# Kernel tuning notes

Measured on AMD Instinct MI355X. Metric: run time of the kernel, lower is better.

The kernel has to match this reference:

```python
import jax, jax.numpy as jnp
import numpy as np

H = 8        # num attention heads
DH = 160     # head dim (hidden_size // H)
HS = 1280    # hidden_size
CAD = 768    # cross_attention_dim
R = 4        # LoRA rank
LORA_SCALE = 1.0  # `scale` forward arg (default 1.0)


def setup_inputs() -> dict:
    key = jax.random.key(0)
    ks = jax.random.split(key, 16)
    rn = lambda k, s, std=0.02: (jax.random.normal(k, s) * std).astype(jnp.float32)
    return {
        "hidden_states": jax.random.normal(ks[0], (8, 4096, HS), jnp.float32),
        "encoder_hidden_states": jax.random.normal(ks[1], (8, 77, CAD), jnp.float32),
        # base attention projections (nn.Linear weight layout: [out, in])
        "Wq": rn(ks[2], (HS, HS)),
        "Wk": rn(ks[3], (HS, CAD)),
        "Wv": rn(ks[4], (HS, CAD)),
        "Wo": rn(ks[5], (HS, HS)),
        "bo": jnp.zeros((HS,), jnp.float32),
        # LoRA down/up pairs (down std ~ 1/rank; up nonzero so grads flow)
        "q_down": rn(ks[6], (R, HS), 0.25), "q_up": rn(ks[7], (HS, R)),
        "k_down": rn(ks[8], (R, CAD), 0.25), "k_up": rn(ks[9], (HS, R)),
        "v_down": rn(ks[10], (R, CAD), 0.25), "v_up": rn(ks[11], (HS, R)),
        "o_down": rn(ks[12], (R, HS), 0.25), "o_up": rn(ks[13], (HS, R)),
    }


def reference(hidden_states, encoder_hidden_states, Wq, Wk, Wv, Wo, bo,
              q_down, q_up, k_down, k_up, v_down, v_up, o_down, o_up):
    B, S, _ = hidden_states.shape
    T = encoder_hidden_states.shape[1]
    lora = lambda x, d, u: (x @ d.T) @ u.T  # LoRALinearLayer: up(down(x))

    q = hidden_states @ Wq.T + LORA_SCALE * lora(hidden_states, q_down, q_up)
    k = encoder_hidden_states @ Wk.T + LORA_SCALE * lora(encoder_hidden_states, k_down, k_up)
    v = encoder_hidden_states @ Wv.T + LORA_SCALE * lora(encoder_hidden_states, v_down, v_up)

    q = q.reshape(B, S, H, DH)
    k = k.reshape(B, T, H, DH)
    v = v.reshape(B, T, H, DH)

    # attn.get_attention_scores: scaled QK^T, softmax (no mask)
    inv_sqrt_d = jnp.asarray(1.0 / np.sqrt(DH), q.dtype)
    scores = jnp.einsum('bshd,bthd->bhst', q, k) * inv_sqrt_d
    probs = jax.nn.softmax(scores, axis=-1)
    o = jnp.einsum('bhst,bthd->bshd', probs, v).reshape(B, S, H * DH)

    # to_out[0] (Linear with bias) + LoRA on the same input; to_out[1] dropout = identity (eval)
    return o @ Wo.T + bo + LORA_SCALE * lora(o, o_down, o_up)
```

## Files before the change

### kernel.cpp

```cpp
#include <hip/hip_runtime.h>
#include <hip/hip_bf16.h>
#include <stdint.h>

typedef short bf16x8 __attribute__((ext_vector_type(8)));
typedef float f32x4 __attribute__((ext_vector_type(4)));

#define DEVI static __device__ __forceinline__

DEVI ushort f2bf(float f) {
  union { float f; uint32_t u; } v; v.f = f;
  uint32_t u = v.u;
  return (ushort)((u + 0x7fffu + ((u >> 16) & 1u)) >> 16);
}

DEVI void gload16(const void* g, void* l) {
  __builtin_amdgcn_global_load_lds((const __attribute__((address_space(1))) void*)g,
                                   (__attribute__((address_space(3))) void*)l,
                                   16, 0, 0);
}

#define SB() __builtin_amdgcn_sched_barrier(0)
#define BAR() __builtin_amdgcn_s_barrier()
#define MFMA(a, b, c) __builtin_amdgcn_mfma_f32_16x16x32_bf16((a), (b), (c), 0, 0, 0)


__global__ void fold_kernel(const float* __restrict__ W, const float* __restrict__ up,
                            const float* __restrict__ down, ushort* __restrict__ out,
                            int OUT, int IN, int transpose, float scale) {
  int idx = blockIdx.x * 256 + threadIdx.x;
  if (idx >= OUT * IN) return;
  int o = idx / IN, i = idx % IN;
  float v = W[idx];
#pragma unroll
  for (int r = 0; r < 4; ++r) v += up[o * 4 + r] * down[r * IN + i];
  v *= scale;
  out[transpose ? ((long)i * OUT + o) : idx] = f2bf(v);
}

__global__ void cvt_kernel(const float* __restrict__ in, ushort* __restrict__ out, int n8) {
  int idx = blockIdx.x * 256 + threadIdx.x;
  if (idx >= n8) return;
  const float4* p = (const float4*)(in + (long)idx * 8);
  float4 a = p[0], b = p[1];
  union { ushort us[8]; uint4 v; } r;
  r.us[0] = f2bf(a.x); r.us[1] = f2bf(a.y); r.us[2] = f2bf(a.z); r.us[3] = f2bf(a.w);
  r.us[4] = f2bf(b.x); r.us[5] = f2bf(b.y); r.us[6] = f2bf(b.z); r.us[7] = f2bf(b.w);
  *(uint4*)(out + (long)idx * 8) = r.v;
}


__global__ __launch_bounds__(256) void gemm_bt(
    const ushort* __restrict__ A, long sA0, long sA1, int lda, int validM,
    const ushort* __restrict__ B, long sB0, long sB1, int ldb, int validN,
    float* __restrict__ C32, ushort* __restrict__ C16, long sC0, long sC1, int ldc,
    const float* __restrict__ bias, int K)
{
  __shared__ ushort As[128 * 32];
  __shared__ ushort Bs[128 * 32];

  const int z = blockIdx.z;
  const ushort* Ab = A + (long)(z >> 3) * sA0 + (long)(z & 7) * sA1;
  const ushort* Bb = B + (long)(z >> 3) * sB0 + (long)(z & 7) * sB1;
  const int m0 = blockIdx.x * 128;
  const int n0 = blockIdx.y * 128;
  const int tid = threadIdx.x;
  const int lane = tid & 63;
  const int wid = tid >> 6;

  const int c0 = tid;
  const int arow0 = min(m0 + (c0 >> 2), validM - 1);
  const int arow1 = min(m0 + (c0 >> 2) + 64, validM - 1);
  const int brow0 = min(n0 + (c0 >> 2), validN - 1);
  const int brow1 = min(n0 + (c0 >> 2) + 64, validN - 1);
  const int seg = (c0 & 3) * 8;

  const int wr = (wid >> 1) * 64;
  const int wc = (wid & 1) * 64;
  const int frow = lane & 15;
  const int fk = (lane >> 4) * 8;

  f32x4 acc[4][4] = {};

  for (int kt = 0; kt < K; kt += 32) {
    gload16(Ab + (long)arow0 * lda + kt + seg, As + c0 * 8);
    gload16(Ab + (long)arow1 * lda + kt + seg, As + (c0 + 256) * 8);
    gload16(Bb + (long)brow0 * ldb + kt + seg, Bs + c0 * 8);
    gload16(Bb + (long)brow1 * ldb + kt + seg, Bs + (c0 + 256) * 8);
    __syncthreads();

    bf16x8 af[4], bfr[4];
#pragma unroll
    for (int m = 0; m < 4; ++m)
      af[m] = *(const bf16x8*)(As + (wr + m * 16 + frow) * 32 + fk);
#pragma unroll
    for (int n = 0; n < 4; ++n)
      bfr[n] = *(const bf16x8*)(Bs + (wc + n * 16 + frow) * 32 + fk);
#pragma unroll
    for (int m = 0; m < 4; ++m)
#pragma unroll
      for (int n = 0; n < 4; ++n)
        acc[m][n] = MFMA(af[m], bfr[n], acc[m][n]);
    __syncthreads();
  }

  const long cb = (long)(z >> 3) * sC0 + (long)(z & 7) * sC1;
  const int crow = m0 + wr + (lane >> 4) * 4;
  const int ccol = n0 + wc + (lane & 15);
#pragma unroll
  for (int m = 0; m < 4; ++m)
#pragma unroll
    for (int n = 0; n < 4; ++n)
#pragma unroll
      for (int j = 0; j < 4; ++j) {
        int r = crow + m * 16 + j;
        int c = ccol + n * 16;
        if (r < validM && c < validN) {
          float v = acc[m][n][j];
          if (bias) v += bias[c];
          if (C32) C32[cb + (long)r * ldc + c] = v;
          else     C16[cb + (long)r * ldc + c] = f2bf(v);
        }
      }
}

__global__ __launch_bounds__(256, 2) void score_softmax(
    const ushort* __restrict__ hsb, const ushort* __restrict__ Mt,
    ushort* __restrict__ probs)
{
  __shared__ ushort lds[40960];

  const int z = blockIdx.z;
  const int s0 = blockIdx.x * 128;
  const int h0 = blockIdx.y * 2;
  const int tid = threadIdx.x;
  const int lane = tid & 63;
  const int wid = tid >> 6;
  const int wM = wid >> 1;
  const int wN = wid & 1;
  const int l15 = lane & 15;
  const int l4 = lane >> 4;
  const int sl = tid & 7;

  const ushort* Ag = hsb + ((long)z * 4096 + s0) * 1280;
  long asrc[4]; int adst[4];
#pragma unroll
  for (int j = 0; j < 4; ++j) {
    int r = j * 32 + (tid >> 3);
    asrc[j] = (long)r * 1280 + ((sl ^ (r & 7)) * 8);
    adst[j] = (j * 256 + tid) * 8;
  }
  const ushort* Bg = Mt + (long)z * (640L * 1280);
  long bsrc[6]; int bdst[6];
#pragma unroll
  for (int j = 0; j < 6; ++j) {
    int rb = j * 32 + (tid >> 3);
    int c = h0 * 96 + rb;
    int hh = c / 96, tt = min(c - hh * 96, 76);
    bsrc[j] = (long)(hh * 77 + tt) * 1280 + ((sl ^ (rb & 7)) * 8);
    bdst[j] = 8192 + (j * 256 + tid) * 8;
  }

  int aoff[2][4], boff[2][6];
#pragma unroll
  for (int kk = 0; kk < 2; ++kk) {
#pragma unroll
    for (int m = 0; m < 4; ++m) {
      int r = wM * 64 + m * 16 + l15;
      aoff[kk][m] = r * 64 + (((kk * 4 + l4) ^ (r & 7)) * 8);
    }
#pragma unroll
    for (int n = 0; n < 6; ++n) {
      int r = wN * 96 + n * 16 + l15;
      boff[kk][n] = 8192 + r * 64 + (((kk * 4 + l4) ^ (r & 7)) * 8);
    }
  }

  f32x4 acc[4][6] = {};

#define SS_STAGE(bb, kt) { \
    _Pragma("unroll") for (int j = 0; j < 4; ++j) gload16(Ag + asrc[j] + (kt), &lds[(bb) + adst[j]]); \
    _Pragma("unroll") for (int j = 0; j < 6; ++j) gload16(Bg + bsrc[j] + (kt), &lds[(bb) + bdst[j]]); }

  SS_STAGE(0, 0)

  for (int t = 0; t < 20; ++t) {
    const int base = (t & 1) * 20480;
    if (t + 1 < 20) {
      SS_STAGE(20480 - base, (t + 1) * 64)
      asm volatile("s_waitcnt vmcnt(10)" ::: "memory");
    } else {
      asm volatile("s_waitcnt vmcnt(0)" ::: "memory");
    }
    SB(); BAR(); SB();
#pragma unroll
    for (int kk = 0; kk < 2; ++kk) {
      bf16x8 av[4], bv[6];
#pragma unroll
      for (int m = 0; m < 4; ++m) av[m] = *(const bf16x8*)(&lds[base + aoff[kk][m]]);
#pragma unroll
      for (int n = 0; n < 6; ++n) bv[n] = *(const bf16x8*)(&lds[base + boff[kk][n]]);
      __builtin_amdgcn_s_setprio(1);
#pragma unroll
      for (int m = 0; m < 4; ++m)
#pragma unroll
        for (int n = 0; n < 6; ++n)
          acc[m][n] = MFMA(av[m], bv[n], acc[m][n]);
      __builtin_amdgcn_s_setprio(0);
    }
    SB(); BAR();
  }
#undef SS_STAGE

#pragma unroll
  for (int m = 0; m < 4; ++m)
#pragma unroll
    for (int j = 0; j < 4; ++j) {
      float mx = -1e30f;
#pragma unroll
      for (int n = 0; n < 6; ++n)
        if (n * 16 + l15 < 77) mx = fmaxf(mx, acc[m][n][j]);
#pragma unroll
      for (int o = 8; o; o >>= 1) mx = fmaxf(mx, __shfl_xor(mx, o));
      float sum = 0.f;
#pragma unroll
      for (int n = 0; n < 6; ++n) {
        float e = (n * 16 + l15 < 77) ? __expf(acc[m][n][j] - mx) : 0.f;
        acc[m][n][j] = e;
        sum += e;
      }
#pragma unroll
      for (int o = 8; o; o >>= 1) sum += __shfl_xor(sum, o);
      float inv = 1.f / sum;
#pragma unroll
      for (int n = 0; n < 6; ++n) acc[m][n][j] *= inv;
    }

  __syncthreads();
  ushort* pw = lds + wid * 5632;
#pragma unroll
  for (int m = 0; m < 4; ++m)
#pragma unroll
    for (int n = 0; n < 5; ++n)
#pragma unroll
      for (int j = 0; j < 4; ++j)
        pw[(m * 16 + l4 * 4 + j) * 88 + n * 16 + l15] = f2bf(acc[m][n][j]);

  const uint* pw32 = (const uint*)pw;
  uint* probs32 = (uint*)probs;
  const int head = h0 + wN;
  const long sbase = (long)z * 4096 + s0 + wM * 64;
#pragma unroll 4
  for (int k = 0; k < 40; ++k) {
    int f2 = k * 64 + lane;
    int r = f2 / 40;
    int tp = f2 - r * 40;
    probs32[(sbase + r) * 320 + head * 40 + tp] = pw32[r * 44 + tp];
  }
}

__global__ __launch_bounds__(256, 2) void gemm_out(
    const ushort* __restrict__ P, const ushort* __restrict__ Nt,
    float* __restrict__ C, const float* __restrict__ bias)
{
  __shared__ ushort lds[32768];

  const int z = blockIdx.z;
  const ushort* Ab = P + (long)z * (4096L * 640) + (long)blockIdx.x * 128 * 640;
  const ushort* Bb = Nt + (long)z * (1280L * 640) + (long)blockIdx.y * 128 * 640;
  const int tid = threadIdx.x;
  const int lane = tid & 63;
  const int wid = tid >> 6;
  const int wM = wid >> 1;
  const int wN = wid & 1;
  const int l15 = lane & 15;
  const int l4 = lane >> 4;
  const int sl = tid & 7;

  long asrc[4]; int adst[4], bdst[4];
#pragma unroll
  for (int j = 0; j < 4; ++j) {
    int r = j * 32 + (tid >> 3);
    asrc[j] = (long)r * 640 + ((sl ^ (r & 7)) * 8);
    adst[j] = (j * 256 + tid) * 8;
    bdst[j] = 8192 + (j * 256 + tid) * 8;
  }

  int aoff[2][4], boff[2][4];
#pragma unroll
  for (int kk = 0; kk < 2; ++kk) {
#pragma unroll
    for (int m = 0; m < 4; ++m) {
      int r = wM * 64 + m * 16 + l15;
      aoff[kk][m] = r * 64 + (((kk * 4 + l4) ^ (r & 7)) * 8);
    }
#pragma unroll
    for (int n = 0; n < 4; ++n) {
      int r = wN * 64 + n * 16 + l15;
      boff[kk][n] = 8192 + r * 64 + (((kk * 4 + l4) ^ (r & 7)) * 8);
    }
  }

  f32x4 acc[4][4] = {};

#define OG_STAGE(bb, kt) { \
    _Pragma("unroll") for (int j = 0; j < 4; ++j) gload16(Ab + asrc[j] + (kt), &lds[(bb) + adst[j]]); \
    _Pragma("unroll") for (int j = 0; j < 4; ++j) gload16(Bb + asrc[j] + (kt), &lds[(bb) + bdst[j]]); }

  OG_STAGE(0, 0)

  for (int t = 0; t < 10; ++t) {
    const int base = (t & 1) * 16384;
    if (t + 1 < 10) {
      OG_STAGE(16384 - base, (t + 1) * 64)
      asm volatile("s_waitcnt vmcnt(8)" ::: "memory");
    } else {
      asm volatile("s_waitcnt vmcnt(0)" ::: "memory");
    }
    SB(); BAR(); SB();
#pragma unroll
    for (int kk = 0; kk < 2; ++kk) {
      bf16x8 av[4], bv[4];
#pragma unroll
      for (int m = 0; m < 4; ++m) av[m] = *(const bf16x8*)(&lds[base + aoff[kk][m]]);
#pragma unroll
      for (int n = 0; n < 4; ++n) bv[n] = *(const bf16x8*)(&lds[base + boff[kk][n]]);
      __builtin_amdgcn_s_setprio(1);
#pragma unroll
      for (int m = 0; m < 4; ++m)
#pragma unroll
        for (int n = 0; n < 4; ++n)
          acc[m][n] = MFMA(av[m], bv[n], acc[m][n]);
      __builtin_amdgcn_s_setprio(0);
    }
    SB(); BAR();
  }
#undef OG_STAGE

  __syncthreads();
  float* pw = (float*)lds + wid * 1088;
  const int ccol = blockIdx.y * 128 + wN * 64;
  const float4 bv4 = *(const float4*)(bias + ccol + l15 * 4);
  const long crow0 = (long)z * 4096 + blockIdx.x * 128 + wM * 64;
#pragma unroll
  for (int m = 0; m < 4; ++m) {
#pragma unroll
    for (int n = 0; n < 4; ++n)
#pragma unroll
      for (int j = 0; j < 4; ++j)
        pw[(l4 * 4 + j) * 68 + n * 16 + l15] = acc[m][n][j];
    asm volatile("s_waitcnt lgkmcnt(0)" ::: "memory"); SB();
#pragma unroll
    for (int pass = 0; pass < 4; ++pass) {
      int r = pass * 4 + l4;
      float4 v = *(const float4*)(pw + r * 68 + l15 * 4);
      v.x += bv4.x; v.y += bv4.y; v.z += bv4.z; v.w += bv4.w;
      *(float4*)(C + (crow0 + m * 16 + r) * 1280 + ccol + l15 * 4) = v;
    }
    asm volatile("s_waitcnt lgkmcnt(0)" ::: "memory"); SB();
  }
}

__global__ void zero_nt_pad(ushort* __restrict__ Nt) {
  int idx = blockIdx.x * 256 + threadIdx.x;
  if (idx >= 8 * 1280 * 24) return;
  int b = idx / (1280 * 24);
  int rem = idx % (1280 * 24);
  int j = rem / 24, q = rem % 24;
  int h = q / 3, t = 77 + q % 3;
  Nt[(long)b * 1280 * 640 + (long)j * 640 + h * 80 + t] = 0;
}

extern "C" void kernel_launch(void* const* d_in, const int* in_sizes, int n_in,
                              void* d_out, int out_size, void* d_ws, size_t ws_size,
                              hipStream_t stream) {
  (void)in_sizes; (void)n_in; (void)out_size; (void)ws_size;
  const float* hs     = (const float*)d_in[0];
  const float* ehs    = (const float*)d_in[1];
  const float* Wq     = (const float*)d_in[2];
  const float* Wk     = (const float*)d_in[3];
  const float* Wv     = (const float*)d_in[4];
  const float* Wo     = (const float*)d_in[5];
  const float* bo     = (const float*)d_in[6];
  const float* q_down = (const float*)d_in[7];
  const float* q_up   = (const float*)d_in[8];
  const float* k_down = (const float*)d_in[9];
  const float* k_up   = (const float*)d_in[10];
  const float* v_down = (const float*)d_in[11];
  const float* v_up   = (const float*)d_in[12];
  const float* o_down = (const float*)d_in[13];
  const float* o_up   = (const float*)d_in[14];

  char* w = (char*)d_ws;
  size_t off = 0;
  auto alloc = [&](size_t b) { char* p = w + off; off = (off + b + 255) & ~(size_t)255; return p; };
  ushort* hs_bf  = (ushort*)alloc(32768L * 1280 * 2);
  ushort* ehs_bf = (ushort*)alloc(616L * 768 * 2);
  ushort* WqT    = (ushort*)alloc(1280L * 1280 * 2);
  ushort* Wkv    = (ushort*)alloc(2560L * 768 * 2);
  ushort* Wo_bf  = (ushort*)alloc(1280L * 1280 * 2);
  ushort* kv_bf  = (ushort*)alloc(616L * 2560 * 2);
  ushort* Mt     = (ushort*)alloc(8L * 640 * 1280 * 2);
  ushort* Nt     = (ushort*)alloc(8L * 1280 * 640 * 2);
  ushort* probs  = (ushort*)alloc(8L * 4096 * 640 * 2);
  float*  outp   = (float*)d_out;
  const float invs = 0.07905694150420949f;

  fold_kernel<<<6400, 256, 0, stream>>>(Wq, q_up, q_down, WqT, 1280, 1280, 1, invs);
  fold_kernel<<<3840, 256, 0, stream>>>(Wk, k_up, k_down, Wkv, 1280, 768, 0, 1.0f);
  fold_kernel<<<3840, 256, 0, stream>>>(Wv, v_up, v_down, Wkv + 1280L * 768, 1280, 768, 0, 1.0f);
  fold_kernel<<<6400, 256, 0, stream>>>(Wo, o_up, o_down, Wo_bf, 1280, 1280, 0, 1.0f);
  cvt_kernel<<<20480, 256, 0, stream>>>(hs, hs_bf, 5242880);
  cvt_kernel<<<231, 256, 0, stream>>>(ehs, ehs_bf, 59136);
  gemm_bt<<<dim3(5, 20, 1), 256, 0, stream>>>(ehs_bf, 0, 0, 768, 616,
      Wkv, 0, 0, 768, 2560, nullptr, kv_bf, 0, 0, 2560, nullptr, 768);
  gemm_bt<<<dim3(1, 10, 64), 256, 0, stream>>>(kv_bf, 77L * 2560, 160, 2560, 77,
      WqT, 0, 160, 1280, 1280, nullptr, Mt, 640L * 1280, 77L * 1280, 1280, nullptr, 160);
  gemm_bt<<<dim3(10, 1, 64), 256, 0, stream>>>(Wo_bf, 0, 160, 1280, 1280,
      kv_bf + 1280, 77L * 2560, 160, 2560, 77, nullptr, Nt, 1280L * 640, 80, 640, nullptr, 160);
  zero_nt_pad<<<960, 256, 0, stream>>>(Nt);
  score_softmax<<<dim3(32, 4, 8), 256, 0, stream>>>(hs_bf, Mt, probs);
  gemm_out<<<dim3(32, 10, 8), 256, 0, stream>>>(probs, Nt, outp, bo);
}
```

Baseline: 286.2 us.

## Fuse prep kernels into one launch and halve K-tile in attention GEMMs

Merges the hidden-state and encoder bf16 conversions, the four LoRA weight folds and the Nt pad zeroing into one block-indexed prep kernel. This removes several small kernel launches and their tail gaps. Separately, score_softmax and gemm_out now stage 32-wide K tiles with a 4-way XOR swizzle instead of 64-wide tiles with 8-way, halving LDS use per block. That may allow more resident blocks, but it doubles the number of barrier-synchronized iterations and shrinks the prefetch depth per stage.

Result: faster. 280.6 us (-2.0%).

```diff
diff --git a/kernel.cpp b/kernel.cpp
--- a/kernel.cpp
+++ b/kernel.cpp
@@ -22,30 +22,62 @@
 #define SB() __builtin_amdgcn_sched_barrier(0)
 #define BAR() __builtin_amdgcn_s_barrier()
 #define MFMA(a, b, c) __builtin_amdgcn_mfma_f32_16x16x32_bf16((a), (b), (c), 0, 0, 0)
-
-
-__global__ void fold_kernel(const float* __restrict__ W, const float* __restrict__ up,
-                            const float* __restrict__ down, ushort* __restrict__ out,
-                            int OUT, int IN, int transpose, float scale) {
-  int idx = blockIdx.x * 256 + threadIdx.x;
-  if (idx >= OUT * IN) return;
-  int o = idx / IN, i = idx % IN;
-  float v = W[idx];
-#pragma unroll
-  for (int r = 0; r < 4; ++r) v += up[o * 4 + r] * down[r * IN + i];
-  v *= scale;
-  out[transpose ? ((long)i * OUT + o) : idx] = f2bf(v);
-}
-
-__global__ void cvt_kernel(const float* __restrict__ in, ushort* __restrict__ out, int n8) {
-  int idx = blockIdx.x * 256 + threadIdx.x;
-  if (idx >= n8) return;
-  const float4* p = (const float4*)(in + (long)idx * 8);
-  float4 a = p[0], b = p[1];
-  union { ushort us[8]; uint4 v; } r;
-  r.us[0] = f2bf(a.x); r.us[1] = f2bf(a.y); r.us[2] = f2bf(a.z); r.us[3] = f2bf(a.w);
-  r.us[4] = f2bf(b.x); r.us[5] = f2bf(b.y); r.us[6] = f2bf(b.z); r.us[7] = f2bf(b.w);
-  *(uint4*)(out + (long)idx * 8) = r.v;
+#define KEY4(r) ((((r) & 3)) ^ (((r) >> 2) & 3))
+
+__global__ __launch_bounds__(256) void prep_fused(
+    const float* __restrict__ hs, ushort* __restrict__ hs_bf,
+    const float* __restrict__ ehs, ushort* __restrict__ ehs_bf,
+    const float* __restrict__ Wq, const float* __restrict__ q_up, const float* __restrict__ q_down,
+    ushort* __restrict__ WqT,
+    const float* __restrict__ Wk, const float* __restrict__ k_up, const float* __restrict__ k_down,
+    const float* __restrict__ Wv, const float* __restrict__ v_up, const float* __restrict__ v_down,
+    ushort* __restrict__ Wkv,
+    const float* __restrict__ Wo, const float* __restrict__ o_up, const float* __restrict__ o_down,
+    ushort* __restrict__ Wo_bf,
+    ushort* __restrict__ Nt, float invs)
+{
+  const int b = blockIdx.x;
+  const int tid = threadIdx.x;
+  if (b < 20480) {
+    long idx = (long)b * 256 + tid;
+    const float4* p = (const float4*)(hs + idx * 8);
+    float4 a = p[0], c = p[1];
+    union { ushort us[8]; uint4 v; } r;
+    r.us[0] = f2bf(a.x); r.us[1] = f2bf(a.y); r.us[2] = f2bf(a.z); r.us[3] = f2bf(a.w);
+    r.us[4] = f2bf(c.x); r.us[5] = f2bf(c.y); r.us[6] = f2bf(c.z); r.us[7] = f2bf(c.w);
+    *(uint4*)(hs_bf + idx * 8) = r.v;
+  } else if (b < 20711) {
+    int idx = (b - 20480) * 256 + tid;
+    if (idx < 59136) {
+      const float4* p = (const float4*)(ehs + (long)idx * 8);
+      float4 a = p[0], c = p[1];
+      union { ushort us[8]; uint4 v; } r;
+      r.us[0] = f2bf(a.x); r.us[1] = f2bf(a.y); r.us[2] = f2bf(a.z); r.us[3] = f2bf(a.w);
+      r.us[4] = f2bf(c.x); r.us[5] = f2bf(c.y); r.us[6] = f2bf(c.z); r.us[7] = f2bf(c.w);
+      *(uint4*)(ehs_bf + (long)idx * 8) = r.v;
+    }
+  } else if (b < 41191) {
+    long f = (long)(b - 20711) * 256 + tid;
+    const float *W, *up, *down; ushort* out;
+    int OUT, IN, transpose; float scale; long base;
+    if (f < 1638400)        { base = f;           W = Wq; up = q_up; down = q_down; out = WqT;   OUT = 1280; IN = 1280; transpose = 1; scale = invs; }
+    else if (f < 2621440)   { base = f - 1638400; W = Wk; up = k_up; down = k_down; out = Wkv;   OUT = 1280; IN = 768;  transpose = 0; scale = 1.f; }
+    else if (f < 3604480)   { base = f - 2621440; W = Wv; up = v_up; down = v_down; out = Wkv + 1280L * 768; OUT = 1280; IN = 768; transpose = 0; scale = 1.f; }
+    else                    { base = f - 3604480; W = Wo; up = o_up; down = o_down; out = Wo_bf; OUT = 1280; IN = 1280; transpose = 0; scale = 1.f; }
+    int o = (int)(base / IN), i = (int)(base % IN);
+    float v = W[base];
+#pragma unroll
+    for (int r = 0; r < 4; ++r) v += up[o * 4 + r] * down[r * IN + i];
+    v *= scale;
+    out[transpose ? ((long)i * OUT + o) : base] = f2bf(v);
+  } else {
+    int idx = (b - 41191) * 256 + tid;
+    int bb = idx / (1280 * 24);
+    int rem = idx % (1280 * 24);
+    int j = rem / 24, q = rem % 24;
+    int h = q / 3, t = 77 + q % 3;
+    Nt[(long)bb * 1280 * 640 + (long)j * 640 + h * 80 + t] = 0;
+  }
 }
 
 
@@ -127,7 +159,7 @@
     const ushort* __restrict__ hsb, const ushort* __restrict__ Mt,
     ushort* __restrict__ probs)
 {
-  __shared__ ushort lds[40960];
+  __shared__ ushort lds[22528];
 
   const int z = blockIdx.z;
   const int s0 = blockIdx.x * 128;
@@ -139,74 +171,68 @@
   const int wN = wid & 1;
   const int l15 = lane & 15;
   const int l4 = lane >> 4;
-  const int sl = tid & 7;
+  const int sl = tid & 3;
 
   const ushort* Ag = hsb + ((long)z * 4096 + s0) * 1280;
-  long asrc[4]; int adst[4];
-#pragma unroll
-  for (int j = 0; j < 4; ++j) {
-    int r = j * 32 + (tid >> 3);
-    asrc[j] = (long)r * 1280 + ((sl ^ (r & 7)) * 8);
+  long asrc[2]; int adst[2];
+#pragma unroll
+  for (int j = 0; j < 2; ++j) {
+    int r = j * 64 + (tid >> 2);
+    asrc[j] = (long)r * 1280 + ((sl ^ KEY4(r)) * 8);
     adst[j] = (j * 256 + tid) * 8;
   }
   const ushort* Bg = Mt + (long)z * (640L * 1280);
-  long bsrc[6]; int bdst[6];
-#pragma unroll
-  for (int j = 0; j < 6; ++j) {
-    int rb = j * 32 + (tid >> 3);
+  long bsrc[3]; int bdst[3];
+#pragma unroll
+  for (int j = 0; j < 3; ++j) {
+    int rb = j * 64 + (tid >> 2);
     int c = h0 * 96 + rb;
     int hh = c / 96, tt = min(c - hh * 96, 76);
-    bsrc[j] = (long)(hh * 77 + tt) * 1280 + ((sl ^ (rb & 7)) * 8);
-    bdst[j] = 8192 + (j * 256 + tid) * 8;
-  }
-
-  int aoff[2][4], boff[2][6];
-#pragma unroll
-  for (int kk = 0; kk < 2; ++kk) {
-#pragma unroll
-    for (int m = 0; m < 4; ++m) {
-      int r = wM * 64 + m * 16 + l15;
-      aoff[kk][m] = r * 64 + (((kk * 4 + l4) ^ (r & 7)) * 8);
-    }
-#pragma unroll
-    for (int n = 0; n < 6; ++n) {
-      int r = wN * 96 + n * 16 + l15;
-      boff[kk][n] = 8192 + r * 64 + (((kk * 4 + l4) ^ (r & 7)) * 8);
-    }
+    bsrc[j] = (long)(hh * 77 + tt) * 1280 + ((sl ^ KEY4(rb)) * 8);
+    bdst[j] = 4096 + (j * 256 + tid) * 8;
+  }
+
+  int aoff[4], boff[6];
+#pragma unroll
+  for (int m = 0; m < 4; ++m) {
+    int r = wM * 64 + m * 16 + l15;
+    aoff[m] = r * 32 + ((l4 ^ KEY4(r)) * 8);
+  }
+#pragma unroll
+  for (int n = 0; n < 6; ++n) {
+    int r = wN * 96 + n * 16 + l15;
+    boff[n] = 4096 + r * 32 + ((l4 ^ KEY4(r)) * 8);
   }
 
   f32x4 acc[4][6] = {};
 
 #define SS_STAGE(bb, kt) { \
-    _Pragma("unroll") for (int j = 0; j < 4; ++j) gload16(Ag + asrc[j] + (kt), &lds[(bb) + adst[j]]); \
-    _Pragma("unroll") for (int j = 0; j < 6; ++j) gload16(Bg + bsrc[j] + (kt), &lds[(bb) + bdst[j]]); }
+    _Pragma("unroll") for (int j = 0; j < 2; ++j) gload16(Ag + asrc[j] + (kt), &lds[(bb) + adst[j]]); \
+    _Pragma("unroll") for (int j = 0; j < 3; ++j) gload16(Bg + bsrc[j] + (kt), &lds[(bb) + bdst[j]]); }
 
   SS_STAGE(0, 0)
 
-  for (int t = 0; t < 20; ++t) {
-    const int base = (t & 1) * 20480;
-    if (t + 1 < 20) {
-      SS_STAGE(20480 - base, (t + 1) * 64)
-      asm volatile("s_waitcnt vmcnt(10)" ::: "memory");
+  for (int t = 0; t < 40; ++t) {
+    const int base = (t & 1) * 10240;
+    if (t + 1 < 40) {
+      SS_STAGE(10240 - base, (t + 1) * 32)
+      asm volatile("s_waitcnt vmcnt(5)" ::: "memory");
     } else {
       asm volatile("s_waitcnt vmcnt(0)" ::: "memory");
     }
     SB(); BAR(); SB();
-#pragma unroll
-    for (int kk = 0; kk < 2; ++kk) {
-      bf16x8 av[4], bv[6];
-#pragma unroll
-      for (int m = 0; m < 4; ++m) av[m] = *(const bf16x8*)(&lds[base + aoff[kk][m]]);
-#pragma unroll
-      for (int n = 0; n < 6; ++n) bv[n] = *(const bf16x8*)(&lds[base + boff[kk][n]]);
-      __builtin_amdgcn_s_setprio(1);
-#pragma unroll
-      for (int m = 0; m < 4; ++m)
-#pragma unroll
-        for (int n = 0; n < 6; ++n)
-          acc[m][n] = MFMA(av[m], bv[n], acc[m][n]);
-      __builtin_amdgcn_s_setprio(0);
-    }
+    bf16x8 av[4], bv[6];
+#pragma unroll
+    for (int m = 0; m < 4; ++m) av[m] = *(const bf16x8*)(&lds[base + aoff[m]]);
+#pragma unroll
+    for (int n = 0; n < 6; ++n) bv[n] = *(const bf16x8*)(&lds[base + boff[n]]);
+    __builtin_amdgcn_s_setprio(1);
+#pragma unroll
+    for (int m = 0; m < 4; ++m)
+#pragma unroll
+      for (int n = 0; n < 6; ++n)
+        acc[m][n] = MFMA(av[m], bv[n], acc[m][n]);
+    __builtin_amdgcn_s_setprio(0);
     SB(); BAR();
   }
 #undef SS_STAGE
@@ -262,7 +288,7 @@
     const ushort* __restrict__ P, const ushort* __restrict__ Nt,
     float* __restrict__ C, const float* __restrict__ bias)
 {
-  __shared__ ushort lds[32768];
+  __shared__ ushort lds[16384];
 
   const int z = blockIdx.z;
   const ushort* Ab = P + (long)z * (4096L * 640) + (long)blockIdx.x * 128 * 640;
@@ -274,64 +300,58 @@
   const int wN = wid & 1;
   const int l15 = lane & 15;
   const int l4 = lane >> 4;
-  const int sl = tid & 7;
-
-  long asrc[4]; int adst[4], bdst[4];
-#pragma unroll
-  for (int j = 0; j < 4; ++j) {
-    int r = j * 32 + (tid >> 3);
-    asrc[j] = (long)r * 640 + ((sl ^ (r & 7)) * 8);
+  const int sl = tid & 3;
+
+  long asrc[2]; int adst[2], bdst[2];
+#pragma unroll
+  for (int j = 0; j < 2; ++j) {
+    int r = j * 64 + (tid >> 2);
+    asrc[j] = (long)r * 640 + ((sl ^ KEY4(r)) * 8);
     adst[j] = (j * 256 + tid) * 8;
-    bdst[j] = 8192 + (j * 256 + tid) * 8;
-  }
-
-  int aoff[2][4], boff[2][4];
-#pragma unroll
-  for (int kk = 0; kk < 2; ++kk) {
-#pragma unroll
-    for (int m = 0; m < 4; ++m) {
-      int r = wM * 64 + m * 16 + l15;
-      aoff[kk][m] = r * 64 + (((kk * 4 + l4) ^ (r & 7)) * 8);
-    }
-#pragma unroll
-    for (int n = 0; n < 4; ++n) {
-      int r = wN * 64 + n * 16 + l15;
-      boff[kk][n] = 8192 + r * 64 + (((kk * 4 + l4) ^ (r & 7)) * 8);
-    }
+    bdst[j] = 4096 + (j * 256 + tid) * 8;
+  }
+
+  int aoff[4], boff[4];
+#pragma unroll
+  for (int m = 0; m < 4; ++m) {
+    int r = wM * 64 + m * 16 + l15;
+    aoff[m] = r * 32 + ((l4 ^ KEY4(r)) * 8);
+  }
+#pragma unroll
+  for (int n = 0; n < 4; ++n) {
+    int r = wN * 64 + n * 16 + l15;
+    boff[n] = 4096 + r * 32 + ((l4 ^ KEY4(r)) * 8);
   }
 
   f32x4 acc[4][4] = {};
 
 #define OG_STAGE(bb, kt) { \
-    _Pragma("unroll") for (int j = 0; j < 4; ++j) gload16(Ab + asrc[j] + (kt), &lds[(bb) + adst[j]]); \
-    _Pragma("unroll") for (int j = 0; j < 4; ++j) gload16(Bb + asrc[j] + (kt), &lds[(bb) + bdst[j]]); }
+    _Pragma("unroll") for (int j = 0; j < 2; ++j) gload16(Ab + asrc[j] + (kt), &lds[(bb) + adst[j]]); \
+    _Pragma("unroll") for (int j = 0; j < 2; ++j) gload16(Bb + asrc[j] + (kt), &lds[(bb) + bdst[j]]); }
 
   OG_STAGE(0, 0)
 
-  for (int t = 0; t < 10; ++t) {
-    const int base = (t & 1) * 16384;
-    if (t + 1 < 10) {
-      OG_STAGE(16384 - base, (t + 1) * 64)
-      asm volatile("s_waitcnt vmcnt(8)" ::: "memory");
+  for (int t = 0; t < 20; ++t) {
+    const int base = (t & 1) * 8192;
+    if (t + 1 < 20) {
+      OG_STAGE(8192 - base, (t + 1) * 32)
+      asm volatile("s_waitcnt vmcnt(4)" ::: "memory");
     } else {
       asm volatile("s_waitcnt vmcnt(0)" ::: "memory");
     }
     SB(); BAR(); SB();
-#pragma unroll
-    for (int kk = 0; kk < 2; ++kk) {
-      bf16x8 av[4], bv[4];
-#pragma unroll
-      for (int m = 0; m < 4; ++m) av[m] = *(const bf16x8*)(&lds[base + aoff[kk][m]]);
-#pragma unroll
-      for (int n = 0; n < 4; ++n) bv[n] = *(const bf16x8*)(&lds[base + boff[kk][n]]);
-      __builtin_amdgcn_s_setprio(1);
-#pragma unroll
-      for (int m = 0; m < 4; ++m)
-#pragma unroll
-        for (int n = 0; n < 4; ++n)
-          acc[m][n] = MFMA(av[m], bv[n], acc[m][n]);
-      __builtin_amdgcn_s_setprio(0);
-    }
+    bf16x8 av[4], bv[4];
+#pragma unroll
+    for (int m = 0; m < 4; ++m) av[m] = *(const bf16x8*)(&lds[base + aoff[m]]);
+#pragma unroll
+    for (int n = 0; n < 4; ++n) bv[n] = *(const bf16x8*)(&lds[base + boff[n]]);
+    __builtin_amdgcn_s_setprio(1);
+#pragma unroll
+    for (int m = 0; m < 4; ++m)
+#pragma unroll
+      for (int n = 0; n < 4; ++n)
+        acc[m][n] = MFMA(av[m], bv[n], acc[m][n]);
+    __builtin_amdgcn_s_setprio(0);
     SB(); BAR();
   }
 #undef OG_STAGE
@@ -358,16 +378,6 @@
     }
     asm volatile("s_waitcnt lgkmcnt(0)" ::: "memory"); SB();
   }
-}
-
-__global__ void zero_nt_pad(ushort* __restrict__ Nt) {
-  int idx = blockIdx.x * 256 + threadIdx.x;
-  if (idx >= 8 * 1280 * 24) return;
-  int b = idx / (1280 * 24);
-  int rem = idx % (1280 * 24);
-  int j = rem / 24, q = rem % 24;
-  int h = q / 3, t = 77 + q % 3;
-  Nt[(long)b * 1280 * 640 + (long)j * 640 + h * 80 + t] = 0;
 }
 
 extern "C" void kernel_launch(void* const* d_in, const int* in_sizes, int n_in,
@@ -405,19 +415,15 @@
   float*  outp   = (float*)d_out;
   const float invs = 0.07905694150420949f;
 
-  fold_kernel<<<6400, 256, 0, stream>>>(Wq, q_up, q_down, WqT, 1280, 1280, 1, invs);
-  fold_kernel<<<3840, 256, 0, stream>>>(Wk, k_up, k_down, Wkv, 1280, 768, 0, 1.0f);
-  fold_kernel<<<3840, 256, 0, stream>>>(Wv, v_up, v_down, Wkv + 1280L * 768, 1280, 768, 0, 1.0f);
-  fold_kernel<<<6400, 256, 0, stream>>>(Wo, o_up, o_down, Wo_bf, 1280, 1280, 0, 1.0f);
-  cvt_kernel<<<20480, 256, 0, stream>>>(hs, hs_bf, 5242880);
-  cvt_kernel<<<231, 256, 0, stream>>>(ehs, ehs_bf, 59136);
+  prep_fused<<<42151, 256, 0, stream>>>(hs, hs_bf, ehs, ehs_bf,
+      Wq, q_up, q_down, WqT, Wk, k_up, k_down, Wv, v_up, v_down, Wkv,
+      Wo, o_up, o_down, Wo_bf, Nt, invs);
   gemm_bt<<<dim3(5, 20, 1), 256, 0, stream>>>(ehs_bf, 0, 0, 768, 616,
       Wkv, 0, 0, 768, 2560, nullptr, kv_bf, 0, 0, 2560, nullptr, 768);
   gemm_bt<<<dim3(1, 10, 64), 256, 0, stream>>>(kv_bf, 77L * 2560, 160, 2560, 77,
       WqT, 0, 160, 1280, 1280, nullptr, Mt, 640L * 1280, 77L * 1280, 1280, nullptr, 160);
   gemm_bt<<<dim3(10, 1, 64), 256, 0, stream>>>(Wo_bf, 0, 160, 1280, 1280,
       kv_bf + 1280, 77L * 2560, 160, 2560, 77, nullptr, Nt, 1280L * 640, 80, 640, nullptr, 160);
-  zero_nt_pad<<<960, 256, 0, stream>>>(Nt);
   score_softmax<<<dim3(32, 4, 8), 256, 0, stream>>>(hs_bf, Mt, probs);
   gemm_out<<<dim3(32, 10, 8), 256, 0, stream>>>(probs, Nt, outp, bo);
 }
```
